# Kernel optimization log

Hardware: AMD Instinct MI355X
Metric: run time of the kernel (lower is better)

Reference implementation:

```python
import jax, jax.numpy as jnp
import numpy as np

NUM_FORMULAS = 1024
INPUT_DIM = 256
BATCH = 2048


def setup_inputs() -> dict:
    key = jax.random.key(0)
    k_x, k_mu, k_sigma = jax.random.split(key, 3)
    inputs = jax.random.normal(k_x, (BATCH, INPUT_DIM), dtype=jnp.float32)
    # keras random_normal initializer default stddev = 0.05
    mu = 0.05 * jax.random.normal(k_mu, (NUM_FORMULAS, INPUT_DIM), dtype=jnp.float32)
    sigma = 0.05 * jax.random.normal(k_sigma, (1, NUM_FORMULAS, INPUT_DIM), dtype=jnp.float32)
    temperature = jnp.float32(2.0)
    return {"inputs": inputs, "mu": mu, "sigma": sigma, "temperature": temperature}


def reference(inputs, mu, sigma, temperature):
    # diff: (batch, num_formulas, dim)
    diff = inputs[:, None, :] - mu[None, :, :]
    # weighted L2 norm over feature dim -> (batch, num_formulas)
    dist = jnp.sqrt(jnp.sum(jnp.square(diff * sigma), axis=-1))
    loc = jnp.exp(-dist)
    # sigmoid-gated temperature, softmax over formulas (last axis)
    return jax.nn.softmax(jax.nn.sigmoid(temperature) * loc, axis=-1)
```

## Files before the change

### kernel.cpp

```cpp
#include <hip/hip_runtime.h>
#include <math.h>

#define NF 1024
#define DIM 256
#define BATCH 2048
#define K 512
#define BMF 16
#define KS 32
#define NSTEP (K / KS)

#define WS_C_OFF (NF * K * 2)

typedef __attribute__((ext_vector_type(8))) short short8;
typedef __attribute__((ext_vector_type(4))) float f32x4;

__device__ __forceinline__ unsigned short f2bf(float f) {
    unsigned u = __float_as_uint(f);
    u += 0x7fffu + ((u >> 16) & 1u);
    return (unsigned short)(u >> 16);
}

__global__ __launch_bounds__(256) void k_prep(const float* __restrict__ mu,
                                              const float* __restrict__ sigma,
                                              uint4* __restrict__ Bb4,
                                              float* __restrict__ c) {
    const int t = threadIdx.x;
    const int f = blockIdx.x * 4 + (t >> 6);
    const int sq = t & 63;
    const float4 mv = *(const float4*)&mu[f * DIM + sq * 4];
    const float4 sv = *(const float4*)&sigma[f * DIM + sq * 4];

    uint4 pk; float cp = 0.f;
    {
        const float s2x = sv.x * sv.x;
        pk.x = (unsigned)f2bf(s2x) | ((unsigned)f2bf(-2.0f * s2x * mv.x) << 16);
        cp += s2x * mv.x * mv.x;
        const float s2y = sv.y * sv.y;
        pk.y = (unsigned)f2bf(s2y) | ((unsigned)f2bf(-2.0f * s2y * mv.y) << 16);
        cp += s2y * mv.y * mv.y;
        const float s2z = sv.z * sv.z;
        pk.z = (unsigned)f2bf(s2z) | ((unsigned)f2bf(-2.0f * s2z * mv.z) << 16);
        cp += s2z * mv.z * mv.z;
        const float s2w = sv.w * sv.w;
        pk.w = (unsigned)f2bf(s2w) | ((unsigned)f2bf(-2.0f * s2w * mv.w) << 16);
        cp += s2w * mv.w * mv.w;
    }
    Bb4[(sq >> 2) * 4096 + (sq & 3) * 1024 + f] = pk;

    #pragma unroll
    for (int off = 32; off > 0; off >>= 1) cp += __shfl_down(cp, off, 64);
    if ((t & 63) == 0) c[f] = cp;
}

__global__ __launch_bounds__(1024, 1) void k_fused(const float* __restrict__ x,
                                                   const ushort* __restrict__ Bb,
                                                   const float* __restrict__ c,
                                                   const float* __restrict__ temp,
                                                   float* __restrict__ out) {
    const int t = threadIdx.x;
    const int w = t >> 6;
    const int lane = t & 63;
    const int m16 = lane & 15;
    const int q = lane >> 4;
    const int r0 = blockIdx.x * BMF;

    __shared__ __align__(16) ushort ldsA[BMF * K];
    __shared__ float wsum[16][BMF];
    __shared__ float rowInv[BMF];

    {
        const int row = t >> 6, kc = t & 63;
        const float4 v = *(const float4*)&x[(r0 + row) * DIM + kc * 4];
        uint4 pk;
        pk.x = (unsigned)f2bf(v.x * v.x) | ((unsigned)f2bf(v.x) << 16);
        pk.y = (unsigned)f2bf(v.y * v.y) | ((unsigned)f2bf(v.y) << 16);
        pk.z = (unsigned)f2bf(v.z * v.z) | ((unsigned)f2bf(v.z) << 16);
        pk.w = (unsigned)f2bf(v.w * v.w) | ((unsigned)f2bf(v.w) << 16);
        *(uint4*)&ldsA[(row * 64 + (kc ^ (row & 7))) * 8] = pk;
    }

    f32x4 acc[4];
    #pragma unroll
    for (int ct = 0; ct < 4; ++ct) acc[ct] = (f32x4){0.f, 0.f, 0.f, 0.f};

    const ushort* bp = Bb + q * (NF * 8) + (w * 64 + m16) * 8;

    short8 bA[4], bB[4];
    #pragma unroll
    for (int ct = 0; ct < 4; ++ct)
        bA[ct] = *(const short8*)(bp + ct * 128);

    __syncthreads();

    #pragma unroll 1
    for (int s = 0; s < NSTEP; s += 2) {
        #pragma unroll
        for (int ct = 0; ct < 4; ++ct)
            bB[ct] = *(const short8*)(bp + (s + 1) * (NF * KS) + ct * 128);
        {
            const int kcq = s * 4 + q;
            const short8 av = *(const short8*)&ldsA[(m16 * 64 + (kcq ^ (m16 & 7))) * 8];
            #pragma unroll
            for (int ct = 0; ct < 4; ++ct)
                acc[ct] = __builtin_amdgcn_mfma_f32_16x16x32_bf16(av, bA[ct], acc[ct], 0, 0, 0);
        }
        if (s + 2 < NSTEP) {
            #pragma unroll
            for (int ct = 0; ct < 4; ++ct)
                bA[ct] = *(const short8*)(bp + (s + 2) * (NF * KS) + ct * 128);
        }
        {
            const int kcq = (s + 1) * 4 + q;
            const short8 av = *(const short8*)&ldsA[(m16 * 64 + (kcq ^ (m16 & 7))) * 8];
            #pragma unroll
            for (int ct = 0; ct < 4; ++ct)
                acc[ct] = __builtin_amdgcn_mfma_f32_16x16x32_bf16(av, bB[ct], acc[ct], 0, 0, 0);
        }
    }

    const float g = 1.0f / (1.0f + __expf(-temp[0]));
    float s4[4] = {0.f, 0.f, 0.f, 0.f};
    #pragma unroll
    for (int ct = 0; ct < 4; ++ct) {
        const float cn = c[w * 64 + ct * 16 + m16];
        #pragma unroll
        for (int i = 0; i < 4; ++i) {
            const float dist2 = acc[ct][i] + cn;
            const float dist = sqrtf(fmaxf(dist2, 0.0f));
            const float p = __expf(g * __expf(-dist));
            acc[ct][i] = p;
            s4[i] += p;
        }
    }
    #pragma unroll
    for (int i = 0; i < 4; ++i) {
        #pragma unroll
        for (int mask = 1; mask < 16; mask <<= 1)
            s4[i] += __shfl_xor(s4[i], mask, 64);
    }
    if (m16 == 0) {
        #pragma unroll
        for (int i = 0; i < 4; ++i) wsum[w][q * 4 + i] = s4[i];
    }
    __syncthreads();
    if (t < BMF) {
        float ssum = 0.f;
        #pragma unroll
        for (int ww = 0; ww < 16; ++ww) ssum += wsum[ww][t];
        rowInv[t] = 1.0f / ssum;
    }
    __syncthreads();

    float inv[4];
    #pragma unroll
    for (int i = 0; i < 4; ++i) inv[i] = rowInv[q * 4 + i];
    #pragma unroll
    for (int ct = 0; ct < 4; ++ct) {
        const int fcol = w * 64 + ct * 16 + m16;
        #pragma unroll
        for (int i = 0; i < 4; ++i)
            out[(r0 + q * 4 + i) * NF + fcol] = acc[ct][i] * inv[i];
    }
}

extern "C" void kernel_launch(void* const* d_in, const int* in_sizes, int n_in,
                              void* d_out, int out_size, void* d_ws, size_t ws_size,
                              hipStream_t stream) {
    const float* x     = (const float*)d_in[0];
    const float* mu    = (const float*)d_in[1];
    const float* sigma = (const float*)d_in[2];
    const float* temp  = (const float*)d_in[3];
    float* out = (float*)d_out;

    char* ws = (char*)d_ws;
    ushort* Bb = (ushort*)ws;
    float*  c  = (float*)(ws + WS_C_OFF);

    k_prep<<<NF / 4, 256, 0, stream>>>(mu, sigma, (uint4*)Bb, c);
    k_fused<<<BATCH / BMF, 1024, 0, stream>>>(x, Bb, c, temp, out);
}
```

Before: 75.41 us.

## Enlarge row tile to 64 and reuse B fragments across 16 column tiles per wave

Raises the batch rows per block from 16 to 64 and rearranges the 16 waves into a 4x4 grid, so each wave computes a 16x256 output tile with 16 accumulators. Each B fragment loaded from global memory is now shared by four times as many batch rows, which cuts global/L2 traffic for the packed mu/sigma operand. The B loads are rotated through a 4-slot register ring interleaved with the MFMAs instead of double-buffered per step. In exchange the grid shrinks to 32 blocks, fewer than the number of CUs, register pressure rises, and there is less latency hiding per load.

```diff
diff --git a/kernel.cpp b/kernel.cpp
--- a/kernel.cpp
+++ b/kernel.cpp
@@ -5,7 +5,7 @@
 #define DIM 256
 #define BATCH 2048
 #define K 512
-#define BMF 16
+#define BMF 64
 #define KS 32
 #define NSTEP (K / KS)
 
@@ -62,14 +62,17 @@
     const int lane = t & 63;
     const int m16 = lane & 15;
     const int q = lane >> 4;
+    const int mw = w >> 2, nw = w & 3;
     const int r0 = blockIdx.x * BMF;
 
     __shared__ __align__(16) ushort ldsA[BMF * K];
-    __shared__ float wsum[16][BMF];
+    __shared__ float wsum[16][16];
     __shared__ float rowInv[BMF];
 
-    {
-        const int row = t >> 6, kc = t & 63;
+    #pragma unroll
+    for (int h = 0; h < 4; ++h) {
+        const int u = h * 1024 + t;
+        const int row = u >> 6, kc = u & 63;
         const float4 v = *(const float4*)&x[(r0 + row) * DIM + kc * 4];
         uint4 pk;
         pk.x = (unsigned)f2bf(v.x * v.x) | ((unsigned)f2bf(v.x) << 16);
@@ -79,50 +82,48 @@
         *(uint4*)&ldsA[(row * 64 + (kc ^ (row & 7))) * 8] = pk;
     }
 
-    f32x4 acc[4];
+    f32x4 acc[16];
     #pragma unroll
-    for (int ct = 0; ct < 4; ++ct) acc[ct] = (f32x4){0.f, 0.f, 0.f, 0.f};
+    for (int ct = 0; ct < 16; ++ct) acc[ct] = (f32x4){0.f, 0.f, 0.f, 0.f};
 
-    const ushort* bp = Bb + q * (NF * 8) + (w * 64 + m16) * 8;
+    const ushort* bp = Bb + q * (NF * 8) + nw * 2048 + m16 * 8;
+    const int ar = mw * 16 + m16;
 
-    short8 bA[4], bB[4];
+    short8 bv[4];
     #pragma unroll
     for (int ct = 0; ct < 4; ++ct)
-        bA[ct] = *(const short8*)(bp + ct * 128);
+        bv[ct] = *(const short8*)(bp + ct * 128);
 
     __syncthreads();
 
     #pragma unroll 1
-    for (int s = 0; s < NSTEP; s += 2) {
+    for (int s = 0; s < NSTEP - 1; ++s) {
+        const int kcq = s * 4 + q;
+        const short8 av = *(const short8*)&ldsA[(ar * 64 + (kcq ^ (ar & 7))) * 8];
         #pragma unroll
-        for (int ct = 0; ct < 4; ++ct)
-            bB[ct] = *(const short8*)(bp + (s + 1) * (NF * KS) + ct * 128);
-        {
-            const int kcq = s * 4 + q;
-            const short8 av = *(const short8*)&ldsA[(m16 * 64 + (kcq ^ (m16 & 7))) * 8];
-            #pragma unroll
-            for (int ct = 0; ct < 4; ++ct)
-                acc[ct] = __builtin_amdgcn_mfma_f32_16x16x32_bf16(av, bA[ct], acc[ct], 0, 0, 0);
+        for (int ct = 0; ct < 16; ++ct) {
+            acc[ct] = __builtin_amdgcn_mfma_f32_16x16x32_bf16(av, bv[ct & 3], acc[ct], 0, 0, 0);
+            const int ns  = (ct < 12) ? s : s + 1;
+            const int nct = (ct < 12) ? ct + 4 : ct - 12;
+            bv[ct & 3] = *(const short8*)(bp + ns * (NF * KS) + nct * 128);
         }
-        if (s + 2 < NSTEP) {
-            #pragma unroll
-            for (int ct = 0; ct < 4; ++ct)
-                bA[ct] = *(const short8*)(bp + (s + 2) * (NF * KS) + ct * 128);
-        }
-        {
-            const int kcq = (s + 1) * 4 + q;
-            const short8 av = *(const short8*)&ldsA[(m16 * 64 + (kcq ^ (m16 & 7))) * 8];
-            #pragma unroll
-            for (int ct = 0; ct < 4; ++ct)
-                acc[ct] = __builtin_amdgcn_mfma_f32_16x16x32_bf16(av, bB[ct], acc[ct], 0, 0, 0);
+    }
+    {
+        const int kcq = (NSTEP - 1) * 4 + q;
+        const short8 av = *(const short8*)&ldsA[(ar * 64 + (kcq ^ (ar & 7))) * 8];
+        #pragma unroll
+        for (int ct = 0; ct < 16; ++ct) {
+            acc[ct] = __builtin_amdgcn_mfma_f32_16x16x32_bf16(av, bv[ct & 3], acc[ct], 0, 0, 0);
+            if (ct < 12)
+                bv[ct & 3] = *(const short8*)(bp + (NSTEP - 1) * (NF * KS) + (ct + 4) * 128);
         }
     }
 
     const float g = 1.0f / (1.0f + __expf(-temp[0]));
     float s4[4] = {0.f, 0.f, 0.f, 0.f};
     #pragma unroll
-    for (int ct = 0; ct < 4; ++ct) {
-        const float cn = c[w * 64 + ct * 16 + m16];
+    for (int ct = 0; ct < 16; ++ct) {
+        const float cn = c[nw * 256 + ct * 16 + m16];
         #pragma unroll
         for (int i = 0; i < 4; ++i) {
             const float dist2 = acc[ct][i] + cn;
@@ -144,22 +145,22 @@
     }
     __syncthreads();
     if (t < BMF) {
-        float ssum = 0.f;
-        #pragma unroll
-        for (int ww = 0; ww < 16; ++ww) ssum += wsum[ww][t];
+        const int b = (t >> 4) * 4, r16 = t & 15;
+        const float ssum = (wsum[b][r16] + wsum[b + 1][r16]) +
+                           (wsum[b + 2][r16] + wsum[b + 3][r16]);
         rowInv[t] = 1.0f / ssum;
     }
     __syncthreads();
 
     float inv[4];
     #pragma unroll
-    for (int i = 0; i < 4; ++i) inv[i] = rowInv[q * 4 + i];
+    for (int i = 0; i < 4; ++i) inv[i] = rowInv[mw * 16 + q * 4 + i];
     #pragma unroll
-    for (int ct = 0; ct < 4; ++ct) {
-        const int fcol = w * 64 + ct * 16 + m16;
+    for (int ct = 0; ct < 16; ++ct) {
+        const int fcol = nw * 256 + ct * 16 + m16;
         #pragma unroll
         for (int i = 0; i < 4; ++i)
-            out[(r0 + q * 4 + i) * NF + fcol] = acc[ct][i] * inv[i];
+            out[(r0 + mw * 16 + q * 4 + i) * NF + fcol] = acc[ct][i] * inv[i];
     }
 }
 
```

New measurement: 107.7 us. 42.9% more time.
